# Kernel optimization log

Hardware: AMD Instinct MI355X
Metric: run time of the kernel (lower is better)

The kernel has to match this reference:

```python
import jax, jax.numpy as jnp
import numpy as np

HIDDEN = 512
NUM_HEADS = 8


def setup_inputs() -> dict:
    key = jax.random.key(0)
    ks = jax.random.split(key, 8)
    Tq, Tk, Cq, Ck, H = 1, 65536, 512, 512, HIDDEN
    s = 1.0 / np.sqrt(H)
    return {
        "Q": jax.random.normal(ks[0], (Tq, Cq), jnp.float32),
        "K": jax.random.normal(ks[1], (Tk, Ck), jnp.float32),
        "Wq": jax.random.normal(ks[2], (H, Cq), jnp.float32) * s,
        "bq": jax.random.normal(ks[3], (H,), jnp.float32) * s,
        "Wk": jax.random.normal(ks[4], (H, Ck), jnp.float32) * s,
        "bk": jax.random.normal(ks[5], (H,), jnp.float32) * s,
        "Wout": jax.random.normal(ks[6], (1, NUM_HEADS), jnp.float32) * 0.3,
        "bout": jax.random.normal(ks[7], (1,), jnp.float32) * 0.3,
    }


def reference(Q, K, Wq, bq, Wk, bk, Wout, bout):
    h = NUM_HEADS
    H = Wq.shape[0]
    d = H // h  # per-head dim
    # linear + ReLU projections
    Ql = jax.nn.relu(Q @ Wq.T + bq)          # [1, H]
    Kl = jax.nn.relu(K @ Wk.T + bk)          # [Tk, H]
    # split into heads (T_q == 1 is required by linear_out)
    Qh = Ql.reshape(h, d)                    # [h, d]
    Kh = Kl.reshape(-1, h, d)                # [Tk, h, d]
    # per-head scores, scaled by sqrt(d_head); dropout rate 0 -> identity
    scores = jnp.einsum('hd,thd->th', Qh, Kh) / (d ** 0.5)  # [Tk, h]
    # learned per-head fusion, then softmax over the T_k axis
    logits = scores @ Wout.T + bout          # [Tk, 1]
    return jax.nn.softmax(logits, axis=0)    # [Tk, 1]
```

## Files before the change

kernel.cpp:

```cpp
#include <hip/hip_runtime.h>
#include <hip/hip_fp16.h>

#define CDIM 512
#define ROWS 65536
#define TPW  16

typedef _Float16 half8  __attribute__((ext_vector_type(8)));
typedef __fp16   fp16x2 __attribute__((ext_vector_type(2)));
typedef float    f32x16 __attribute__((ext_vector_type(16)));

__device__ __forceinline__ half8 cvt8(float4 f0, float4 f1) {
    union { fp16x2 h2[4]; half8 h8; } u;
    u.h2[0] = __builtin_amdgcn_cvt_pkrtz(f0.x, f0.y);
    u.h2[1] = __builtin_amdgcn_cvt_pkrtz(f0.z, f0.w);
    u.h2[2] = __builtin_amdgcn_cvt_pkrtz(f1.x, f1.y);
    u.h2[3] = __builtin_amdgcn_cvt_pkrtz(f1.z, f1.w);
    return u.h8;
}

__global__ void prep_kernel(const float* __restrict__ Q, const float* __restrict__ Wq,
                            const float* __restrict__ bq, const float* __restrict__ Wout,
                            const float* __restrict__ Wk,
                            float* __restrict__ v, _Float16* __restrict__ Wkf) {
    __shared__ float qs[CDIM];
    const int t = threadIdx.x;
    if (blockIdx.x < 32) {
        qs[t] = Q[t]; qs[t + 256] = Q[t + 256];
        __syncthreads();
        const int jj  = t >> 4;
        const int sub = t & 15;
        const int j   = blockIdx.x * 16 + jj;
        const float4* w4 = (const float4*)(Wq + (size_t)j * CDIM + sub * 32);
        const float4* q4 = (const float4*)(qs + sub * 32);
        float s = 0.f;
        #pragma unroll
        for (int i = 0; i < 8; ++i) {
            float4 w = w4[i]; float4 q = q4[i];
            s = fmaf(w.x, q.x, s); s = fmaf(w.y, q.y, s);
            s = fmaf(w.z, q.z, s); s = fmaf(w.w, q.w, s);
        }
        s += __shfl_xor(s, 1); s += __shfl_xor(s, 2);
        s += __shfl_xor(s, 4); s += __shfl_xor(s, 8);
        if (sub == 0) {
            s += bq[j];
            s = fmaxf(s, 0.f);
            v[j] = s * Wout[j >> 6] * 0.125f;
        }
    } else {
        const int gid = (blockIdx.x - 32) * 256 + t;
        const int jb  = gid >> 11;
        const int kc  = (gid >> 6) & 31;
        const int l   = gid & 63;
        const int j   = jb * 32 + (l & 31);
        const int k   = kc * 16 + (l >> 5) * 8;
        const float* src = Wk + (size_t)j * CDIM + k;
        float4 f0 = *(const float4*)(src);
        float4 f1 = *(const float4*)(src + 4);
        *(half8*)(Wkf + (size_t)gid * 8) = cvt8(f0, f1);
    }
}

__global__ __launch_bounds__(256, 1) void score_kernel(
    const float* __restrict__ Kmat, const _Float16* __restrict__ Wkf,
    const float* __restrict__ bk, const float* __restrict__ v,
    float* __restrict__ partial2)
{
    __shared__ alignas(16) char fragbuf[2][32768];
    __shared__ float scratch2[2][4][32];

    const int tid  = threadIdx.x;
    const int lane = tid & 63;
    const int wave = tid >> 6;
    const int l31  = lane & 31;
    const int lhi  = lane >> 5;

    const int bid      = blockIdx.x;
    const int cls      = (bid >> 3) & 1;
    const int rowblock = (bid & 7) * 16 + (bid >> 4);
    const int rowbase  = rowblock * (TPW * 32);
    float* pbase = partial2 + (size_t)cls * ROWS;

    half8 B0[32], B1[32];
    {
        const half8* b0 = (const half8*)Wkf + (size_t)(cls * 8 + wave) * 2048 + lane;
        const half8* b1 = (const half8*)Wkf + (size_t)(cls * 8 + 4 + wave) * 2048 + lane;
        #pragma unroll
        for (int kc = 0; kc < 32; ++kc) { B0[kc] = b0[kc * 64]; B1[kc] = b1[kc * 64]; }
    }
    const int j0 = (cls * 8 + wave) * 32 + l31;
    const int j1 = (cls * 8 + 4 + wave) * 32 + l31;
    const float bj0 = bk[j0], vj0 = v[j0];
    const float bj1 = bk[j1], vj1 = v[j1];

    const int srow = lane & 31;
    const int skof = (lane >> 5) * 8;

    {
        const float* g0 = Kmat + (size_t)(rowbase + srow) * CDIM + skof;
        #pragma unroll
        for (int q = 0; q < 4; ++q) {
            #pragma unroll
            for (int h = 0; h < 2; ++h) {
                const int kc = q * 8 + h * 4 + wave;
                float4 f0 = *(const float4*)(g0 + kc * 16);
                float4 f1 = *(const float4*)(g0 + kc * 16 + 4);
                *(half8*)(&fragbuf[0][kc * 1024 + lane * 16]) = cvt8(f0, f1);
            }
        }
    }

    float4 L[2][4];
    {
        const float* g1 = Kmat + (size_t)(rowbase + 32 + srow) * CDIM + skof;
        L[0][0] = *(const float4*)(g1 + wave * 16);
        L[0][1] = *(const float4*)(g1 + wave * 16 + 4);
        L[0][2] = *(const float4*)(g1 + (4 + wave) * 16);
        L[0][3] = *(const float4*)(g1 + (4 + wave) * 16 + 4);
    }
    __syncthreads();

    for (int t = 0; t < TPW; ++t) {
        const int cur = t & 1;
        const bool pf = (t + 1 < TPW);
        const char* sb = fragbuf[cur];
        char* db = fragbuf[cur ^ 1];
        const float* gt = Kmat + (size_t)(rowbase + (t + 1) * 32 + srow) * CDIM + skof;

        if (t > 0 && tid < 32) {
            const int pt = (t - 1) & 1;
            float s = scratch2[pt][0][tid] + scratch2[pt][1][tid]
                    + scratch2[pt][2][tid] + scratch2[pt][3][tid];
            pbase[rowbase + (t - 1) * 32 + tid] = s;
        }

        f32x16 acc0, acc1;
        #pragma unroll
        for (int r = 0; r < 16; ++r) { acc0[r] = 0.f; acc1[r] = 0.f; }

        #pragma unroll
        for (int q = 0; q < 4; ++q) {
            if (pf && q < 3) {
                const int kcA = (q + 1) * 8 + wave;
                const int kcB = (q + 1) * 8 + 4 + wave;
                L[(q + 1) & 1][0] = *(const float4*)(gt + kcA * 16);
                L[(q + 1) & 1][1] = *(const float4*)(gt + kcA * 16 + 4);
                L[(q + 1) & 1][2] = *(const float4*)(gt + kcB * 16);
                L[(q + 1) & 1][3] = *(const float4*)(gt + kcB * 16 + 4);
            }
            __builtin_amdgcn_sched_barrier(0);
            #pragma unroll
            for (int i = 0; i < 8; ++i) {
                const int kc = q * 8 + i;
                half8 a = *(const half8*)(sb + kc * 1024 + lane * 16);
                acc0 = __builtin_amdgcn_mfma_f32_32x32x16_f16(a, B0[kc], acc0, 0, 0, 0);
                acc1 = __builtin_amdgcn_mfma_f32_32x32x16_f16(a, B1[kc], acc1, 0, 0, 0);
            }
            if (pf) {
                const int kcA = q * 8 + wave;
                const int kcB = q * 8 + 4 + wave;
                *(half8*)(db + kcA * 1024 + lane * 16) = cvt8(L[q & 1][0], L[q & 1][1]);
                *(half8*)(db + kcB * 1024 + lane * 16) = cvt8(L[q & 1][2], L[q & 1][3]);
            }
            __builtin_amdgcn_sched_barrier(0);
        }

        if (t + 2 < TPW) {
            const float* gn = gt + 32 * CDIM;
            L[0][0] = *(const float4*)(gn + wave * 16);
            L[0][1] = *(const float4*)(gn + wave * 16 + 4);
            L[0][2] = *(const float4*)(gn + (4 + wave) * 16);
            L[0][3] = *(const float4*)(gn + (4 + wave) * 16 + 4);
        }
        __builtin_amdgcn_sched_barrier(0);

        {
            float part[16];
            #pragma unroll
            for (int r = 0; r < 16; ++r)
                part[r] = fmaxf(acc0[r] + bj0, 0.f) * vj0 + fmaxf(acc1[r] + bj1, 0.f) * vj1;

            float q0[8];
            #pragma unroll
            for (int i = 0; i < 8; ++i) {
                const bool b = lane & 1;
                float keep = b ? part[i + 8] : part[i];
                float send = b ? part[i] : part[i + 8];
                q0[i] = keep + __shfl_xor(send, 1);
            }
            float q1[4];
            #pragma unroll
            for (int i = 0; i < 4; ++i) {
                const bool b = lane & 2;
                float keep = b ? q0[i + 4] : q0[i];
                float send = b ? q0[i] : q0[i + 4];
                q1[i] = keep + __shfl_xor(send, 2);
            }
            float q2[2];
            #pragma unroll
            for (int i = 0; i < 2; ++i) {
                const bool b = lane & 4;
                float keep = b ? q1[i + 2] : q1[i];
                float send = b ? q1[i] : q1[i + 2];
                q2[i] = keep + __shfl_xor(send, 4);
            }
            float q3;
            {
                const bool b = lane & 8;
                float keep = b ? q2[1] : q2[0];
                float send = b ? q2[0] : q2[1];
                q3 = keep + __shfl_xor(send, 8);
            }
            float s = q3 + __shfl_xor(q3, 16);
            if (l31 < 16) {
                const int rr  = ((l31 & 1) << 3) | ((l31 & 2) << 1) | ((l31 & 4) >> 1) | ((l31 & 8) >> 3);
                const int row = (rr & 3) + 8 * (rr >> 2) + 4 * lhi;
                scratch2[cur][wave][row] = s;
            }
        }

        __syncthreads();
    }

    if (tid < 32) {
        const int pt = (TPW - 1) & 1;
        float s = scratch2[pt][0][tid] + scratch2[pt][1][tid]
                + scratch2[pt][2][tid] + scratch2[pt][3][tid];
        pbase[rowbase + (TPW - 1) * 32 + tid] = s;
    }
}

__global__ void expsum_kernel(const float* __restrict__ partial2, float* __restrict__ logits,
                              float* __restrict__ blocksum) {
    __shared__ float red[256];
    const int t = threadIdx.x;
    const int row = blockIdx.x * 256 + t;
    const float lg = partial2[row] + partial2[ROWS + row];
    logits[row] = lg;
    red[t] = expf(lg);
    __syncthreads();
    for (int s = 128; s > 0; s >>= 1) {
        if (t < s) red[t] += red[t + s];
        __syncthreads();
    }
    if (t == 0) blocksum[blockIdx.x] = red[0];
}

__global__ void norm_kernel(const float* __restrict__ logits, const float* __restrict__ blocksum,
                            float* __restrict__ out) {
    __shared__ float red[256];
    const int t = threadIdx.x;
    red[t] = blocksum[t];
    __syncthreads();
    for (int s = 128; s > 0; s >>= 1) {
        if (t < s) red[t] += red[t + s];
        __syncthreads();
    }
    const float zinv = 1.0f / red[0];
    const int i = blockIdx.x * 256 + t;
    out[i] = expf(logits[i]) * zinv;
}

extern "C" void kernel_launch(void* const* d_in, const int* in_sizes, int n_in,
                              void* d_out, int out_size, void* d_ws, size_t ws_size,
                              hipStream_t stream) {
    const float* Q    = (const float*)d_in[0];
    const float* Kmat = (const float*)d_in[1];
    const float* Wq   = (const float*)d_in[2];
    const float* bq   = (const float*)d_in[3];
    const float* Wk   = (const float*)d_in[4];
    const float* bk   = (const float*)d_in[5];
    const float* Wout = (const float*)d_in[6];
    float* out = (float*)d_out;

    char* ws = (char*)d_ws;
    _Float16* Wkf   = (_Float16*)(ws);
    float* v        = (float*)(ws + 524288);
    float* partial2 = (float*)(ws + 526336);
    float* logits   = (float*)(ws + 1050624);
    float* blocksum = (float*)(ws + 1312768);

    hipLaunchKernelGGL(prep_kernel,   dim3(160),  dim3(256), 0, stream, Q, Wq, bq, Wout, Wk, v, Wkf);
    hipLaunchKernelGGL(score_kernel,  dim3(256),  dim3(256), 0, stream, Kmat, Wkf, bk, v, partial2);
    hipLaunchKernelGGL(expsum_kernel, dim3(256),  dim3(256), 0, stream, partial2, logits, blocksum);
    hipLaunchKernelGGL(norm_kernel,   dim3(256),  dim3(256), 0, stream, logits, blocksum, out);
}
```

Baseline: 61.90 us.

## Restructure score GEMM into LDS-tiled 256x256 blocks with streamed Wk tiles

Replaces the register-resident Wk slab design (each block holding 256 output columns in registers and iterating 16 row tiles) with a classic tiled GEMM. Each 512-thread block computes a 256-row by 256-column tile, double-buffering both the fp16-converted K tile and the Wk tile in LDS, with Wk loaded via global_load_lds. The change aims to raise MFMA reuse per LDS read through a 4x2 accumulator block per wave and to use more waves per CU. In exchange it streams Wk from memory for every block instead of once per block, uses more LDS, and carries larger accumulator register pressure.

Measured after the change: 71.58 us. 15.6% more time.

```diff
diff --git a/kernel.cpp b/kernel.cpp
--- a/kernel.cpp
+++ b/kernel.cpp
@@ -3,11 +3,15 @@
 
 #define CDIM 512
 #define ROWS 65536
-#define TPW  16
+#define BM   256
 
 typedef _Float16 half8  __attribute__((ext_vector_type(8)));
 typedef __fp16   fp16x2 __attribute__((ext_vector_type(2)));
 typedef float    f32x16 __attribute__((ext_vector_type(16)));
+
+#define GLD_LDS16(gp, lp) __builtin_amdgcn_global_load_lds( \
+    (const __attribute__((address_space(1))) unsigned int*)(gp), \
+    (__attribute__((address_space(3))) unsigned int*)(lp), 16, 0, 0)
 
 __device__ __forceinline__ half8 cvt8(float4 f0, float4 f1) {
     union { fp16x2 h2[4]; half8 h8; } u;
@@ -60,172 +64,149 @@
     }
 }
 
-__global__ __launch_bounds__(256, 1) void score_kernel(
+__global__ __launch_bounds__(512, 1) void score_kernel(
     const float* __restrict__ Kmat, const _Float16* __restrict__ Wkf,
     const float* __restrict__ bk, const float* __restrict__ v,
     float* __restrict__ partial2)
 {
-    __shared__ alignas(16) char fragbuf[2][32768];
-    __shared__ float scratch2[2][4][32];
+    __shared__ alignas(16) char Ab[2][32768];
+    __shared__ alignas(16) char Bbuf[2][32768];
+    __shared__ float scr[2][4][128];
 
     const int tid  = threadIdx.x;
     const int lane = tid & 63;
     const int wave = tid >> 6;
     const int l31  = lane & 31;
     const int lhi  = lane >> 5;
-
-    const int bid      = blockIdx.x;
-    const int cls      = (bid >> 3) & 1;
-    const int rowblock = (bid & 7) * 16 + (bid >> 4);
-    const int rowbase  = rowblock * (TPW * 32);
-    float* pbase = partial2 + (size_t)cls * ROWS;
-
-    half8 B0[32], B1[32];
-    {
-        const half8* b0 = (const half8*)Wkf + (size_t)(cls * 8 + wave) * 2048 + lane;
-        const half8* b1 = (const half8*)Wkf + (size_t)(cls * 8 + 4 + wave) * 2048 + lane;
-        #pragma unroll
-        for (int kc = 0; kc < 32; ++kc) { B0[kc] = b0[kc * 64]; B1[kc] = b1[kc * 64]; }
-    }
-    const int j0 = (cls * 8 + wave) * 32 + l31;
-    const int j1 = (cls * 8 + 4 + wave) * 32 + l31;
+    const int wm   = wave >> 2;
+    const int wn   = wave & 3;
+    const int cls  = blockIdx.y;
+    const int rowbase = blockIdx.x * BM;
+
+    const float* gA = Kmat + (size_t)(rowbase + wave * 32 + l31) * CDIM + lhi * 8;
+    const _Float16* gB = Wkf + ((size_t)(cls * 8 + wave) * 32) * 512;
+
+    f32x16 acc[4][2];
+    #pragma unroll
+    for (int mb = 0; mb < 4; ++mb)
+        #pragma unroll
+        for (int b = 0; b < 2; ++b)
+            #pragma unroll
+            for (int r = 0; r < 16; ++r) acc[mb][b][r] = 0.f;
+
+    #pragma unroll
+    for (int kc = 0; kc < 4; ++kc) {
+        float4 f0 = *(const float4*)(gA + kc * 16);
+        float4 f1 = *(const float4*)(gA + kc * 16 + 4);
+        *(half8*)(Ab[0] + (wave * 4 + kc) * 1024 + lane * 16) = cvt8(f0, f1);
+        GLD_LDS16(gB + (size_t)kc * 512 + lane * 8, Bbuf[0] + (wave * 4 + kc) * 1024);
+    }
+    float4 R[4][2];
+    #pragma unroll
+    for (int kc = 0; kc < 4; ++kc) {
+        R[kc][0] = *(const float4*)(gA + 64 + kc * 16);
+        R[kc][1] = *(const float4*)(gA + 64 + kc * 16 + 4);
+    }
+    __syncthreads();
+
+    #pragma unroll
+    for (int ks = 0; ks < 8; ++ks) {
+        const int cur = ks & 1;
+        if (ks < 7) {
+            #pragma unroll
+            for (int kc = 0; kc < 4; ++kc) {
+                *(half8*)(Ab[cur ^ 1] + (wave * 4 + kc) * 1024 + lane * 16)
+                    = cvt8(R[kc][0], R[kc][1]);
+                GLD_LDS16(gB + (size_t)((ks + 1) * 4 + kc) * 512 + lane * 8,
+                          Bbuf[cur ^ 1] + (wave * 4 + kc) * 1024);
+            }
+        }
+        if (ks < 6) {
+            #pragma unroll
+            for (int kc = 0; kc < 4; ++kc) {
+                R[kc][0] = *(const float4*)(gA + (ks + 2) * 64 + kc * 16);
+                R[kc][1] = *(const float4*)(gA + (ks + 2) * 64 + kc * 16 + 4);
+            }
+        }
+        __builtin_amdgcn_sched_barrier(0);
+        #pragma unroll
+        for (int kc = 0; kc < 4; ++kc) {
+            half8 a0 = *(const half8*)(Ab[cur] + ((wm * 4 + 0) * 4 + kc) * 1024 + lane * 16);
+            half8 a1 = *(const half8*)(Ab[cur] + ((wm * 4 + 1) * 4 + kc) * 1024 + lane * 16);
+            half8 a2 = *(const half8*)(Ab[cur] + ((wm * 4 + 2) * 4 + kc) * 1024 + lane * 16);
+            half8 a3 = *(const half8*)(Ab[cur] + ((wm * 4 + 3) * 4 + kc) * 1024 + lane * 16);
+            half8 b0 = *(const half8*)(Bbuf[cur] + ((wn * 2 + 0) * 4 + kc) * 1024 + lane * 16);
+            half8 b1 = *(const half8*)(Bbuf[cur] + ((wn * 2 + 1) * 4 + kc) * 1024 + lane * 16);
+            acc[0][0] = __builtin_amdgcn_mfma_f32_32x32x16_f16(a0, b0, acc[0][0], 0, 0, 0);
+            acc[1][0] = __builtin_amdgcn_mfma_f32_32x32x16_f16(a1, b0, acc[1][0], 0, 0, 0);
+            acc[2][0] = __builtin_amdgcn_mfma_f32_32x32x16_f16(a2, b0, acc[2][0], 0, 0, 0);
+            acc[3][0] = __builtin_amdgcn_mfma_f32_32x32x16_f16(a3, b0, acc[3][0], 0, 0, 0);
+            acc[0][1] = __builtin_amdgcn_mfma_f32_32x32x16_f16(a0, b1, acc[0][1], 0, 0, 0);
+            acc[1][1] = __builtin_amdgcn_mfma_f32_32x32x16_f16(a1, b1, acc[1][1], 0, 0, 0);
+            acc[2][1] = __builtin_amdgcn_mfma_f32_32x32x16_f16(a2, b1, acc[2][1], 0, 0, 0);
+            acc[3][1] = __builtin_amdgcn_mfma_f32_32x32x16_f16(a3, b1, acc[3][1], 0, 0, 0);
+        }
+        __syncthreads();
+    }
+
+    const int j0 = (cls * 8 + wn * 2 + 0) * 32 + l31;
+    const int j1 = (cls * 8 + wn * 2 + 1) * 32 + l31;
     const float bj0 = bk[j0], vj0 = v[j0];
     const float bj1 = bk[j1], vj1 = v[j1];
 
-    const int srow = lane & 31;
-    const int skof = (lane >> 5) * 8;
-
-    {
-        const float* g0 = Kmat + (size_t)(rowbase + srow) * CDIM + skof;
-        #pragma unroll
-        for (int q = 0; q < 4; ++q) {
-            #pragma unroll
-            for (int h = 0; h < 2; ++h) {
-                const int kc = q * 8 + h * 4 + wave;
-                float4 f0 = *(const float4*)(g0 + kc * 16);
-                float4 f1 = *(const float4*)(g0 + kc * 16 + 4);
-                *(half8*)(&fragbuf[0][kc * 1024 + lane * 16]) = cvt8(f0, f1);
-            }
-        }
-    }
-
-    float4 L[2][4];
-    {
-        const float* g1 = Kmat + (size_t)(rowbase + 32 + srow) * CDIM + skof;
-        L[0][0] = *(const float4*)(g1 + wave * 16);
-        L[0][1] = *(const float4*)(g1 + wave * 16 + 4);
-        L[0][2] = *(const float4*)(g1 + (4 + wave) * 16);
-        L[0][3] = *(const float4*)(g1 + (4 + wave) * 16 + 4);
-    }
-    __syncthreads();
-
-    for (int t = 0; t < TPW; ++t) {
-        const int cur = t & 1;
-        const bool pf = (t + 1 < TPW);
-        const char* sb = fragbuf[cur];
-        char* db = fragbuf[cur ^ 1];
-        const float* gt = Kmat + (size_t)(rowbase + (t + 1) * 32 + srow) * CDIM + skof;
-
-        if (t > 0 && tid < 32) {
-            const int pt = (t - 1) & 1;
-            float s = scratch2[pt][0][tid] + scratch2[pt][1][tid]
-                    + scratch2[pt][2][tid] + scratch2[pt][3][tid];
-            pbase[rowbase + (t - 1) * 32 + tid] = s;
-        }
-
-        f32x16 acc0, acc1;
-        #pragma unroll
-        for (int r = 0; r < 16; ++r) { acc0[r] = 0.f; acc1[r] = 0.f; }
-
-        #pragma unroll
-        for (int q = 0; q < 4; ++q) {
-            if (pf && q < 3) {
-                const int kcA = (q + 1) * 8 + wave;
-                const int kcB = (q + 1) * 8 + 4 + wave;
-                L[(q + 1) & 1][0] = *(const float4*)(gt + kcA * 16);
-                L[(q + 1) & 1][1] = *(const float4*)(gt + kcA * 16 + 4);
-                L[(q + 1) & 1][2] = *(const float4*)(gt + kcB * 16);
-                L[(q + 1) & 1][3] = *(const float4*)(gt + kcB * 16 + 4);
-            }
-            __builtin_amdgcn_sched_barrier(0);
-            #pragma unroll
-            for (int i = 0; i < 8; ++i) {
-                const int kc = q * 8 + i;
-                half8 a = *(const half8*)(sb + kc * 1024 + lane * 16);
-                acc0 = __builtin_amdgcn_mfma_f32_32x32x16_f16(a, B0[kc], acc0, 0, 0, 0);
-                acc1 = __builtin_amdgcn_mfma_f32_32x32x16_f16(a, B1[kc], acc1, 0, 0, 0);
-            }
-            if (pf) {
-                const int kcA = q * 8 + wave;
-                const int kcB = q * 8 + 4 + wave;
-                *(half8*)(db + kcA * 1024 + lane * 16) = cvt8(L[q & 1][0], L[q & 1][1]);
-                *(half8*)(db + kcB * 1024 + lane * 16) = cvt8(L[q & 1][2], L[q & 1][3]);
-            }
-            __builtin_amdgcn_sched_barrier(0);
-        }
-
-        if (t + 2 < TPW) {
-            const float* gn = gt + 32 * CDIM;
-            L[0][0] = *(const float4*)(gn + wave * 16);
-            L[0][1] = *(const float4*)(gn + wave * 16 + 4);
-            L[0][2] = *(const float4*)(gn + (4 + wave) * 16);
-            L[0][3] = *(const float4*)(gn + (4 + wave) * 16 + 4);
-        }
-        __builtin_amdgcn_sched_barrier(0);
-
+    #pragma unroll
+    for (int mb = 0; mb < 4; ++mb) {
+        float part[16];
+        #pragma unroll
+        for (int r = 0; r < 16; ++r)
+            part[r] = fmaxf(acc[mb][0][r] + bj0, 0.f) * vj0
+                    + fmaxf(acc[mb][1][r] + bj1, 0.f) * vj1;
+
+        float q0[8];
+        #pragma unroll
+        for (int i = 0; i < 8; ++i) {
+            const bool b = lane & 1;
+            float keep = b ? part[i + 8] : part[i];
+            float send = b ? part[i] : part[i + 8];
+            q0[i] = keep + __shfl_xor(send, 1);
+        }
+        float q1[4];
+        #pragma unroll
+        for (int i = 0; i < 4; ++i) {
+            const bool b = lane & 2;
+            float keep = b ? q0[i + 4] : q0[i];
+            float send = b ? q0[i] : q0[i + 4];
+            q1[i] = keep + __shfl_xor(send, 2);
+        }
+        float q2[2];
+        #pragma unroll
+        for (int i = 0; i < 2; ++i) {
+            const bool b = lane & 4;
+            float keep = b ? q1[i + 2] : q1[i];
+            float send = b ? q1[i] : q1[i + 2];
+            q2[i] = keep + __shfl_xor(send, 4);
+        }
+        float q3;
         {
-            float part[16];
-            #pragma unroll
-            for (int r = 0; r < 16; ++r)
-                part[r] = fmaxf(acc0[r] + bj0, 0.f) * vj0 + fmaxf(acc1[r] + bj1, 0.f) * vj1;
-
-            float q0[8];
-            #pragma unroll
-            for (int i = 0; i < 8; ++i) {
-                const bool b = lane & 1;
-                float keep = b ? part[i + 8] : part[i];
-                float send = b ? part[i] : part[i + 8];
-                q0[i] = keep + __shfl_xor(send, 1);
-            }
-            float q1[4];
-            #pragma unroll
-            for (int i = 0; i < 4; ++i) {
-                const bool b = lane & 2;
-                float keep = b ? q0[i + 4] : q0[i];
-                float send = b ? q0[i] : q0[i + 4];
-                q1[i] = keep + __shfl_xor(send, 2);
-            }
-            float q2[2];
-            #pragma unroll
-            for (int i = 0; i < 2; ++i) {
-                const bool b = lane & 4;
-                float keep = b ? q1[i + 2] : q1[i];
-                float send = b ? q1[i] : q1[i + 2];
-                q2[i] = keep + __shfl_xor(send, 4);
-            }
-            float q3;
-            {
-                const bool b = lane & 8;
-                float keep = b ? q2[1] : q2[0];
-                float send = b ? q2[0] : q2[1];
-                q3 = keep + __shfl_xor(send, 8);
-            }
-            float s = q3 + __shfl_xor(q3, 16);
-            if (l31 < 16) {
-                const int rr  = ((l31 & 1) << 3) | ((l31 & 2) << 1) | ((l31 & 4) >> 1) | ((l31 & 8) >> 3);
-                const int row = (rr & 3) + 8 * (rr >> 2) + 4 * lhi;
-                scratch2[cur][wave][row] = s;
-            }
-        }
-
-        __syncthreads();
-    }
-
-    if (tid < 32) {
-        const int pt = (TPW - 1) & 1;
-        float s = scratch2[pt][0][tid] + scratch2[pt][1][tid]
-                + scratch2[pt][2][tid] + scratch2[pt][3][tid];
-        pbase[rowbase + (TPW - 1) * 32 + tid] = s;
+            const bool b = lane & 8;
+            float keep = b ? q2[1] : q2[0];
+            float send = b ? q2[0] : q2[1];
+            q3 = keep + __shfl_xor(send, 8);
+        }
+        float s = q3 + __shfl_xor(q3, 16);
+        if (l31 < 16) {
+            const int rr  = ((l31 & 1) << 3) | ((l31 & 2) << 1) | ((l31 & 4) >> 1) | ((l31 & 8) >> 3);
+            const int row = (rr & 3) + 8 * (rr >> 2) + 4 * lhi;
+            scr[wm][wn][mb * 32 + row] = s;
+        }
+    }
+    __syncthreads();
+
+    if (tid < 256) {
+        const int wmx = tid >> 7;
+        const int idx = tid & 127;
+        float s = scr[wmx][0][idx] + scr[wmx][1][idx] + scr[wmx][2][idx] + scr[wmx][3][idx];
+        partial2[(size_t)cls * ROWS + rowbase + wmx * 128 + idx] = s;
     }
 }
 
@@ -279,8 +260,8 @@
     float* logits   = (float*)(ws + 1050624);
     float* blocksum = (float*)(ws + 1312768);
 
-    hipLaunchKernelGGL(prep_kernel,   dim3(160),  dim3(256), 0, stream, Q, Wq, bq, Wout, Wk, v, Wkf);
-    hipLaunchKernelGGL(score_kernel,  dim3(256),  dim3(256), 0, stream, Kmat, Wkf, bk, v, partial2);
-    hipLaunchKernelGGL(expsum_kernel, dim3(256),  dim3(256), 0, stream, partial2, logits, blocksum);
-    hipLaunchKernelGGL(norm_kernel,   dim3(256),  dim3(256), 0, stream, logits, blocksum, out);
-}
+    hipLaunchKernelGGL(prep_kernel,   dim3(160),     dim3(256), 0, stream, Q, Wq, bq, Wout, Wk, v, Wkf);
+    hipLaunchKernelGGL(score_kernel,  dim3(256, 2),  dim3(512), 0, stream, Kmat, Wkf, bk, v, partial2);
+    hipLaunchKernelGGL(expsum_kernel, dim3(256),     dim3(256), 0, stream, partial2, logits, blocksum);
+    hipLaunchKernelGGL(norm_kernel,   dim3(256),     dim3(256), 0, stream, logits, blocksum, out);
+}
```

## Prefetch whole next K tile into registers one iteration ahead

Applied to the files above, without the earlier changes.

Replaces the quarter-by-quarter interleaved global-load / LDS-store pipeline with a full-tile register prefetch. All 16 float4 loads for tile t+2 are issued after the MFMA loop, and the previous tile is converted and stored to LDS only after all MFMAs finish. This gives the loads a full iteration of latency slack and lets the MFMA loop run uninterrupted. In exchange it uses more VGPRs (L grows from 8 to 16 float4) and serializes the LDS stores after compute, which could lower occupancy or expose store latency.

Result: slower. 72.77 us (+17.6%).

```diff
diff --git a/kernel.cpp b/kernel.cpp
--- a/kernel.cpp
+++ b/kernel.cpp
@@ -94,37 +94,28 @@
 
     const int srow = lane & 31;
     const int skof = (lane >> 5) * 8;
-
-    {
-        const float* g0 = Kmat + (size_t)(rowbase + srow) * CDIM + skof;
-        #pragma unroll
-        for (int q = 0; q < 4; ++q) {
-            #pragma unroll
-            for (int h = 0; h < 2; ++h) {
-                const int kc = q * 8 + h * 4 + wave;
-                float4 f0 = *(const float4*)(g0 + kc * 16);
-                float4 f1 = *(const float4*)(g0 + kc * 16 + 4);
-                *(half8*)(&fragbuf[0][kc * 1024 + lane * 16]) = cvt8(f0, f1);
-            }
-        }
-    }
-
-    float4 L[2][4];
-    {
-        const float* g1 = Kmat + (size_t)(rowbase + 32 + srow) * CDIM + skof;
-        L[0][0] = *(const float4*)(g1 + wave * 16);
-        L[0][1] = *(const float4*)(g1 + wave * 16 + 4);
-        L[0][2] = *(const float4*)(g1 + (4 + wave) * 16);
-        L[0][3] = *(const float4*)(g1 + (4 + wave) * 16 + 4);
+    const float* gbase = Kmat + (size_t)(rowbase + srow) * CDIM + skof;
+
+    #pragma unroll
+    for (int i = 0; i < 8; ++i) {
+        const int kc = (i >> 1) * 8 + (i & 1) * 4 + wave;
+        float4 f0 = *(const float4*)(gbase + kc * 16);
+        float4 f1 = *(const float4*)(gbase + kc * 16 + 4);
+        *(half8*)(&fragbuf[0][kc * 1024 + lane * 16]) = cvt8(f0, f1);
+    }
+    float4 L[8][2];
+    #pragma unroll
+    for (int i = 0; i < 8; ++i) {
+        const int kc = (i >> 1) * 8 + (i & 1) * 4 + wave;
+        L[i][0] = *(const float4*)(gbase + 32 * CDIM + kc * 16);
+        L[i][1] = *(const float4*)(gbase + 32 * CDIM + kc * 16 + 4);
     }
     __syncthreads();
 
     for (int t = 0; t < TPW; ++t) {
         const int cur = t & 1;
-        const bool pf = (t + 1 < TPW);
         const char* sb = fragbuf[cur];
         char* db = fragbuf[cur ^ 1];
-        const float* gt = Kmat + (size_t)(rowbase + (t + 1) * 32 + srow) * CDIM + skof;
 
         if (t > 0 && tid < 32) {
             const int pt = (t - 1) & 1;
@@ -138,38 +129,31 @@
         for (int r = 0; r < 16; ++r) { acc0[r] = 0.f; acc1[r] = 0.f; }
 
         #pragma unroll
-        for (int q = 0; q < 4; ++q) {
-            if (pf && q < 3) {
-                const int kcA = (q + 1) * 8 + wave;
-                const int kcB = (q + 1) * 8 + 4 + wave;
-                L[(q + 1) & 1][0] = *(const float4*)(gt + kcA * 16);
-                L[(q + 1) & 1][1] = *(const float4*)(gt + kcA * 16 + 4);
-                L[(q + 1) & 1][2] = *(const float4*)(gt + kcB * 16);
-                L[(q + 1) & 1][3] = *(const float4*)(gt + kcB * 16 + 4);
-            }
-            __builtin_amdgcn_sched_barrier(0);
+        for (int kc = 0; kc < 32; kc += 2) {
+            half8 a0 = *(const half8*)(sb + kc * 1024 + lane * 16);
+            half8 a1 = *(const half8*)(sb + (kc + 1) * 1024 + lane * 16);
+            acc0 = __builtin_amdgcn_mfma_f32_32x32x16_f16(a0, B0[kc], acc0, 0, 0, 0);
+            acc1 = __builtin_amdgcn_mfma_f32_32x32x16_f16(a0, B1[kc], acc1, 0, 0, 0);
+            acc0 = __builtin_amdgcn_mfma_f32_32x32x16_f16(a1, B0[kc + 1], acc0, 0, 0, 0);
+            acc1 = __builtin_amdgcn_mfma_f32_32x32x16_f16(a1, B1[kc + 1], acc1, 0, 0, 0);
+        }
+        __builtin_amdgcn_sched_barrier(0);
+
+        if (t + 1 < TPW) {
             #pragma unroll
             for (int i = 0; i < 8; ++i) {
-                const int kc = q * 8 + i;
-                half8 a = *(const half8*)(sb + kc * 1024 + lane * 16);
-                acc0 = __builtin_amdgcn_mfma_f32_32x32x16_f16(a, B0[kc], acc0, 0, 0, 0);
-                acc1 = __builtin_amdgcn_mfma_f32_32x32x16_f16(a, B1[kc], acc1, 0, 0, 0);
-            }
-            if (pf) {
-                const int kcA = q * 8 + wave;
-                const int kcB = q * 8 + 4 + wave;
-                *(half8*)(db + kcA * 1024 + lane * 16) = cvt8(L[q & 1][0], L[q & 1][1]);
-                *(half8*)(db + kcB * 1024 + lane * 16) = cvt8(L[q & 1][2], L[q & 1][3]);
-            }
-            __builtin_amdgcn_sched_barrier(0);
-        }
-
+                const int kc = (i >> 1) * 8 + (i & 1) * 4 + wave;
+                *(half8*)(db + kc * 1024 + lane * 16) = cvt8(L[i][0], L[i][1]);
+            }
+        }
         if (t + 2 < TPW) {
-            const float* gn = gt + 32 * CDIM;
-            L[0][0] = *(const float4*)(gn + wave * 16);
-            L[0][1] = *(const float4*)(gn + wave * 16 + 4);
-            L[0][2] = *(const float4*)(gn + (4 + wave) * 16);
-            L[0][3] = *(const float4*)(gn + (4 + wave) * 16 + 4);
+            const float* gt = gbase + (size_t)(t + 2) * 32 * CDIM;
+            #pragma unroll
+            for (int i = 0; i < 8; ++i) {
+                const int kc = (i >> 1) * 8 + (i & 1) * 4 + wave;
+                L[i][0] = *(const float4*)(gt + kc * 16);
+                L[i][1] = *(const float4*)(gt + kc * 16 + 4);
+            }
         }
         __builtin_amdgcn_sched_barrier(0);
 
```
